# Kernel optimization log

Measured on AMD Instinct MI355X. Metric: run time of the kernel, lower is better.

## Reference

```python
import jax, jax.numpy as jnp
import numpy as np

B, N, D, RNN, K_TOPK = 32, 2000, 128, 640, 64


def setup_inputs() -> dict:
    key = jax.random.key(0)
    ks = jax.random.split(key, 16)
    s = 1.0 / np.sqrt(D)
    return {
        "Ahat": jax.random.uniform(ks[0], (B, N, N), dtype=jnp.float32),
        "node_embs": jax.random.normal(ks[1], (B, N, D), dtype=jnp.float32),
        "ht": jax.random.normal(ks[2], (B, RNN), dtype=jnp.float32),
        "prev_D": jax.random.normal(ks[3], (B, D, D), dtype=jnp.float32) * s,
        "mapper_w": jax.random.normal(ks[4], (D, RNN), dtype=jnp.float32) / np.sqrt(RNN),
        "mapper_b": jnp.zeros((D,), jnp.float32),
        "Wu": jax.random.normal(ks[5], (D, D), jnp.float32) * s,
        "Uu": jax.random.normal(ks[6], (D, D), jnp.float32) * s,
        "bu": jnp.zeros((D, D), jnp.float32),
        "Wr": jax.random.normal(ks[7], (D, D), jnp.float32) * s,
        "Ur": jax.random.normal(ks[8], (D, D), jnp.float32) * s,
        "br": jnp.zeros((D, D), jnp.float32),
        "Wh": jax.random.normal(ks[9], (D, D), jnp.float32) * s,
        "Uh": jax.random.normal(ks[10], (D, D), jnp.float32) * s,
        "bh": jnp.zeros((D, D), jnp.float32),
        "static_w": jax.random.normal(ks[11], (D, D), jnp.float32) * s,
    }


def _gate(W, U, b, x, h, act):
    # W,U: [D,D]; x,h: [B,D,D]; bias broadcasts over batch
    return act(jnp.einsum('ij,bjk->bik', W, x) + jnp.einsum('ij,bjk->bik', U, h) + b)


def reference(Ahat, node_embs, ht, prev_D, mapper_w, mapper_b,
              Wu, Uu, bu, Wr, Ur, br, Wh, Uh, bh, static_w):
    act = jax.nn.relu
    # ---- TopK_with_h ----
    scorer = jnp.tanh(jax.lax.stop_gradient(ht) @ mapper_w.T + mapper_b)     # [B,D]
    scores = jnp.einsum('bnd,bd->bn', node_embs, scorer)                      # [B,N]
    scores = scores / jnp.linalg.norm(scorer, axis=1, keepdims=True)
    _, topk_idx = jax.lax.top_k(scores, K_TOPK)                               # [B,K_TOPK]
    rep = D // K_TOPK + 1
    idx = jnp.tile(topk_idx, (1, rep))[:, :D]                                 # [B,D] selected node ids
    sel = jnp.take_along_axis(node_embs, idx[:, :, None], axis=1)             # [B,D,Dfeat]
    sel = sel * jnp.tanh(jnp.take_along_axis(scores, idx, axis=1))[..., None]
    logp = jax.nn.log_softmax(scores, axis=1)
    p = jnp.exp(logp)
    entropy = -(p * logp).sum(axis=1)                                         # [B]
    policy_score = jnp.take_along_axis(logp, idx, axis=1).mean(axis=1)        # [B]
    x = sel.transpose(0, 2, 1)                                                # [B,Dfeat,D]
    # ---- mat_GRU_cell: evolve GCN weights ----
    update = _gate(Wu, Uu, bu, x, prev_D, jax.nn.sigmoid)
    reset = _gate(Wr, Ur, br, x, prev_D, jax.nn.sigmoid)
    htilda = _gate(Wh, Uh, bh, x, reset * prev_D, jnp.tanh)
    Dw = (1.0 - update) * prev_D + update * htilda                            # [B,D,D]
    # ---- gather selected subgraph ----
    ne = jnp.take_along_axis(node_embs, idx[:, :, None], axis=1)              # [B,D,Dfeat]
    A = jnp.take_along_axis(Ahat, idx[:, :, None], axis=1)                    # [B,D,N]
    A = jnp.take_along_axis(A, idx[:, None, :], axis=2)                       # [B,D,D]
    di = A.sum(axis=1) ** -0.5                                                # [B,D]
    A = di[:, None, :] * A * jax.lax.stop_gradient(di[:, :, None])
    # ---- GCN with evolved + static weights ----
    h1 = act(jnp.einsum('bkj,bjd->bkd', A, jnp.einsum('bjd,bde->bje', ne, Dw)))
    h2 = act(jnp.einsum('bkj,bjd->bkd', A, jnp.einsum('bjd,de->bje', h1, static_w)))
    out = (h1 + h2) * 0.5                                                     # [B,D,Dfeat]
    return (out, policy_score, scorer, entropy)
```

## Files before the change

kernel.cpp:

```cpp
#include <hip/hip_runtime.h>
#include <math.h>


namespace {
constexpr int B_ = 32;
constexpr int N_ = 2000;
constexpr int D_ = 128;
constexpr int R_ = 640;

constexpr size_t OFF_SCORER = 0;
constexpr size_t OFF_INVN   = 4096;
constexpr size_t OFF_CANDV  = 4128;
constexpr size_t OFF_CANDI  = 20512;
constexpr size_t OFF_STATS  = 36896;
constexpr size_t OFF_TKI    = 37664;
constexpr size_t OFF_T0     = 39712;
constexpr size_t OFF_NE0T   = 41760;
constexpr size_t OFF_A0R    = 303904;
constexpr size_t OFF_DW     = 434976;
constexpr size_t OFF_H1     = 959264;

__global__ __launch_bounds__(1024) void k1_scorer(
    const float* __restrict__ ht, const float* __restrict__ mw,
    const float* __restrict__ mb, float* __restrict__ scorer,
    float* __restrict__ invn, float* __restrict__ outScorer) {
  const int b = blockIdx.x, t = threadIdx.x;
  const int d = t & 127, slice = t >> 7;
  __shared__ float sh[R_];
  __shared__ float part[8][128];
  __shared__ float red[2];
  for (int j = t; j < R_; j += 1024) sh[j] = ht[b * R_ + j];
  __syncthreads();
  const float* wp = mw + (size_t)d * R_ + slice * 80;
  const float* hh = sh + slice * 80;
  float acc = 0.f;
  #pragma unroll
  for (int j = 0; j < 80; j += 4) {
    float4 wv = *reinterpret_cast<const float4*>(wp + j);
    acc += wv.x * hh[j] + wv.y * hh[j + 1] + wv.z * hh[j + 2] + wv.w * hh[j + 3];
  }
  part[slice][d] = acc;
  __syncthreads();
  if (t < 128) {
    float a = mb[t];
    #pragma unroll
    for (int s = 0; s < 8; ++s) a += part[s][t];
    const float sv = tanhf(a);
    scorer[b * D_ + t] = sv;
    outScorer[b * D_ + t] = sv;
    float ss = sv * sv;
    #pragma unroll
    for (int o = 32; o > 0; o >>= 1) ss += __shfl_down(ss, o);
    if ((t & 63) == 0) red[t >> 6] = ss;
  }
  __syncthreads();
  if (t == 0) invn[b] = 1.0f / sqrtf(red[0] + red[1]);
}

__global__ __launch_bounds__(256) void k2_scores(
    const float* __restrict__ node, const float* __restrict__ scorer,
    const float* __restrict__ invn, float* __restrict__ cand_v,
    int* __restrict__ cand_i, float* __restrict__ stats) {
  const int b = blockIdx.x, c = blockIdx.y, t = threadIdx.x;
  const int lane = t & 63, w = t >> 6;
  __shared__ float sc[D_];
  __shared__ float cv[256];
  __shared__ int ci[256];
  __shared__ float r1[4], r2[4];
  if (t < D_) sc[t] = scorer[b * D_ + t];
  __syncthreads();
  const float inv = invn[b];
  const int n = c * 250 + t;
  const bool valid = t < 250;
  float v = -INFINITY;
  if (valid) {
    const float* row = node + ((size_t)b * N_ + n) * D_;
    float acc = 0.f;
    for (int j = 0; j < D_; j += 4) {
      float4 a = *reinterpret_cast<const float4*>(row + j);
      acc += a.x * sc[j] + a.y * sc[j + 1] + a.z * sc[j + 2] + a.w * sc[j + 3];
    }
    v = acc * inv;
  }
  float m = v;
  #pragma unroll
  for (int o = 32; o > 0; o >>= 1) m = fmaxf(m, __shfl_xor(m, o));
  if (lane == 0) r1[w] = m;
  __syncthreads();
  const float Mc = fmaxf(fmaxf(r1[0], r1[1]), fmaxf(r1[2], r1[3]));
  __syncthreads();
  float se = 0.f, sx = 0.f;
  if (valid) {
    const float x = v - Mc;
    const float e = expf(x);
    se = e;
    sx = x * e;
  }
  #pragma unroll
  for (int o = 32; o > 0; o >>= 1) {
    se += __shfl_xor(se, o);
    sx += __shfl_xor(sx, o);
  }
  if (lane == 0) { r1[w] = se; r2[w] = sx; }
  cv[t] = v;
  ci[t] = valid ? n : 0x7fffffff;
  __syncthreads();
  if (t == 0) {
    float* st = stats + ((size_t)b * 8 + c) * 3;
    st[0] = Mc;
    st[1] = r1[0] + r1[1] + r1[2] + r1[3];
    st[2] = r2[0] + r2[1] + r2[2] + r2[3];
  }
  const float mv = cv[t];
  const int mi = ci[t];
  int rank = 0;
  for (int j = 0; j < 256; ++j) {
    const float jv = cv[j];
    const int ji = ci[j];
    rank += (jv > mv || (jv == mv && ji < mi)) ? 1 : 0;
  }
  if (valid && rank < 64) {
    cand_v[((size_t)b * 8 + c) * 64 + rank] = mv;
    cand_i[((size_t)b * 8 + c) * 64 + rank] = mi;
  }
}

__global__ __launch_bounds__(512) void k3_merge(
    const float* __restrict__ cand_v, const int* __restrict__ cand_i,
    const float* __restrict__ stats, const float* __restrict__ node,
    int* __restrict__ tki, float* __restrict__ t0v,
    float* __restrict__ outPolicy, float* __restrict__ outEntropy,
    float* __restrict__ ne0T) {
  const int b = blockIdx.x, t = threadIdx.x;
  __shared__ float cv[512];
  __shared__ int ci[512];
  __shared__ float sv[64];
  __shared__ int si[64];
  __shared__ float lne[64][132];
  cv[t] = cand_v[(size_t)b * 512 + t];
  ci[t] = cand_i[(size_t)b * 512 + t];
  __syncthreads();
  {
    const float mv = cv[t];
    const int mi = ci[t];
    int rank = 0;
    for (int j = 0; j < 512; ++j) {
      const float jv = cv[j];
      const int ji = ci[j];
      rank += (jv > mv || (jv == mv && ji < mi)) ? 1 : 0;
    }
    if (rank < 64) { sv[rank] = mv; si[rank] = mi; }
  }
  __syncthreads();
  if (t < 64) {
    tki[b * 64 + t] = si[t];
    const float v = sv[t];
    t0v[b * 64 + t] = tanhf(v);
    float s = v;
    #pragma unroll
    for (int o = 32; o > 0; o >>= 1) s += __shfl_xor(s, o);
    if (t == 0) {
      float M = -INFINITY;
      for (int c = 0; c < 8; ++c) M = fmaxf(M, stats[((size_t)b * 8 + c) * 3]);
      float se = 0.f, sx = 0.f;
      for (int c = 0; c < 8; ++c) {
        const float* st = stats + ((size_t)b * 8 + c) * 3;
        const float f = expf(st[0] - M);
        se += f * st[1];
        sx += f * (st[2] + (st[0] - M) * st[1]);
      }
      const float logS = logf(se);
      outPolicy[b] = s * (1.0f / 64.0f) - M - logS;
      outEntropy[b] = logS - sx / se;
    }
  }
  __syncthreads();
  {
    const int k = t >> 3, q = t & 7;
    const float* src = node + ((size_t)b * N_ + si[k]) * D_ + q * 16;
    #pragma unroll
    for (int j = 0; j < 16; j += 4)
      *reinterpret_cast<float4*>(&lne[k][q * 16 + j]) =
          *reinterpret_cast<const float4*>(src + j);
  }
  __syncthreads();
  {
    const int f = t >> 2, kh = (t & 3) * 16;
    float* dst = ne0T + ((size_t)b * D_ + f) * 64 + kh;
    #pragma unroll
    for (int j = 0; j < 16; j += 4) {
      float4 vv;
      vv.x = lne[kh + j][f];
      vv.y = lne[kh + j + 1][f];
      vv.z = lne[kh + j + 2][f];
      vv.w = lne[kh + j + 3][f];
      *reinterpret_cast<float4*>(dst + j) = vv;
    }
  }
}

__global__ __launch_bounds__(256) void k4_agather(
    const float* __restrict__ Ahat, const int* __restrict__ tki,
    float* __restrict__ A0r) {
  const int b = blockIdx.x, y = blockIdx.y, t = threadIdx.x;
  __shared__ int idx[64];
  if (t < 64) idx[t] = tki[b * 64 + t];
  __syncthreads();
  const int row = y * 4 + (t >> 6);
  const int col = t & 63;
  A0r[(size_t)b * 4096 + row * 64 + col] =
      Ahat[(size_t)b * N_ * N_ + (size_t)idx[row] * N_ + idx[col]];
}

__global__ __launch_bounds__(256) void k5_gru(
    const float* __restrict__ Wu, const float* __restrict__ Uu, const float* __restrict__ bu,
    const float* __restrict__ Wr, const float* __restrict__ Ur, const float* __restrict__ br,
    const float* __restrict__ Wh, const float* __restrict__ Uh, const float* __restrict__ bh,
    const float* __restrict__ ne0T, const float* __restrict__ t0v,
    const float* __restrict__ P, float* __restrict__ Dw) {
  const int b = blockIdx.x, c = blockIdx.y;
  const int t = threadIdx.x, tx = t & 15, ty = t >> 4;
  __shared__ float Wt[16][132], Ut[16][132];
  __shared__ float Xt[16][17], Yt[16][17];
  __shared__ float gs[2][128][17];
  __shared__ float t0s[16];
  const int col = c * 16 + tx;
  const int kq = col & 63;
  if (t < 16) t0s[t] = t0v[b * 64 + (c & 3) * 16 + t];
  const float* neT = ne0T + (size_t)b * D_ * 64;
  const float* Pb = P + (size_t)b * D_ * D_;
  for (int z = 0; z < 2; ++z) {
    const float* W = z ? Wr : Wu;
    const float* U = z ? Ur : Uu;
    const float* bb = z ? br : bu;
    float acc[8] = {};
    for (int f0 = 0; f0 < D_; f0 += 16) {
      __syncthreads();
      #pragma unroll
      for (int rr = 0; rr < 8; rr++) {
        const int i = rr * 16 + ty;
        Wt[tx][i] = W[i * D_ + f0 + tx];
        Ut[tx][i] = U[i * D_ + f0 + tx];
      }
      Xt[ty][tx] = neT[(f0 + ty) * 64 + kq] * t0s[tx];
      Yt[ty][tx] = Pb[(f0 + ty) * D_ + col];
      __syncthreads();
      #pragma unroll
      for (int ff = 0; ff < 16; ff++) {
        const float xv = Xt[ff][tx];
        const float yv = Yt[ff][tx];
        const float4 wa = *reinterpret_cast<const float4*>(&Wt[ff][ty * 8]);
        const float4 wb = *reinterpret_cast<const float4*>(&Wt[ff][ty * 8 + 4]);
        const float4 ua = *reinterpret_cast<const float4*>(&Ut[ff][ty * 8]);
        const float4 ub = *reinterpret_cast<const float4*>(&Ut[ff][ty * 8 + 4]);
        acc[0] += wa.x * xv + ua.x * yv;
        acc[1] += wa.y * xv + ua.y * yv;
        acc[2] += wa.z * xv + ua.z * yv;
        acc[3] += wa.w * xv + ua.w * yv;
        acc[4] += wb.x * xv + ub.x * yv;
        acc[5] += wb.y * xv + ub.y * yv;
        acc[6] += wb.z * xv + ub.z * yv;
        acc[7] += wb.w * xv + ub.w * yv;
      }
    }
    #pragma unroll
    for (int r = 0; r < 8; r++) {
      const int i = ty * 8 + r;
      const float zz = acc[r] + bb[i * D_ + col];
      gs[z][i][tx] = 1.f / (1.f + expf(-zz));
    }
  }
  float acc[8] = {};
  for (int f0 = 0; f0 < D_; f0 += 16) {
    __syncthreads();
    #pragma unroll
    for (int rr = 0; rr < 8; rr++) {
      const int i = rr * 16 + ty;
      Wt[tx][i] = Wh[i * D_ + f0 + tx];
      Ut[tx][i] = Uh[i * D_ + f0 + tx];
    }
    Xt[ty][tx] = neT[(f0 + ty) * 64 + kq] * t0s[tx];
    Yt[ty][tx] = gs[1][f0 + ty][tx] * Pb[(f0 + ty) * D_ + col];
    __syncthreads();
    #pragma unroll
    for (int ff = 0; ff < 16; ff++) {
      const float xv = Xt[ff][tx];
      const float yv = Yt[ff][tx];
      const float4 wa = *reinterpret_cast<const float4*>(&Wt[ff][ty * 8]);
      const float4 wb = *reinterpret_cast<const float4*>(&Wt[ff][ty * 8 + 4]);
      const float4 ua = *reinterpret_cast<const float4*>(&Ut[ff][ty * 8]);
      const float4 ub = *reinterpret_cast<const float4*>(&Ut[ff][ty * 8 + 4]);
      acc[0] += wa.x * xv + ua.x * yv;
      acc[1] += wa.y * xv + ua.y * yv;
      acc[2] += wa.z * xv + ua.z * yv;
      acc[3] += wa.w * xv + ua.w * yv;
      acc[4] += wb.x * xv + ub.x * yv;
      acc[5] += wb.y * xv + ub.y * yv;
      acc[6] += wb.z * xv + ub.z * yv;
      acc[7] += wb.w * xv + ub.w * yv;
    }
  }
  #pragma unroll
  for (int r = 0; r < 8; r++) {
    const int i = ty * 8 + r;
    const size_t off = ((size_t)b * D_ + i) * D_ + col;
    const float hh = tanhf(acc[r] + bh[i * D_ + col]);
    const float uu = gs[0][i][tx];
    const float pp = Pb[i * D_ + col];
    Dw[off] = (1.f - uu) * pp + uu * hh;
  }
}

__global__ __launch_bounds__(256) void k6_gcn1(
    const float* __restrict__ ne0T, const float* __restrict__ Dw,
    const float* __restrict__ A0r, float* __restrict__ h1ws) {
  const int b = blockIdx.x, c = blockIdx.y;
  const int t = threadIdx.x, tx = t & 15, ty = t >> 4;
  __shared__ float As[64][68];
  __shared__ float di[64];
  __shared__ float At[16][68];
  __shared__ float Bt[16][36];
  __shared__ float Ts[64][36];
  const float* Ab = A0r + (size_t)b * 4096;
  const float* neT = ne0T + (size_t)b * D_ * 64;
  const float* Db = Dw + (size_t)b * D_ * D_;
  #pragma unroll
  for (int ph = 0; ph < 4; ++ph) {
    const int i = ph * 16 + ty;
    *reinterpret_cast<float4*>(&As[i][tx * 4]) =
        *reinterpret_cast<const float4*>(Ab + i * 64 + tx * 4);
  }
  __syncthreads();
  if (t < 64) {
    float s = 0.f;
    #pragma unroll
    for (int i = 0; i < 64; ++i) s += As[i][t];
    di[t] = 1.0f / sqrtf(2.0f * s);
  }
  __syncthreads();
  #pragma unroll
  for (int ph = 0; ph < 4; ++ph) {
    const int i = ph * 16 + ty;
    const float sI = 2.0f * di[i];
    float4 v = *reinterpret_cast<float4*>(&As[i][tx * 4]);
    v.x *= sI * di[tx * 4];
    v.y *= sI * di[tx * 4 + 1];
    v.z *= sI * di[tx * 4 + 2];
    v.w *= sI * di[tx * 4 + 3];
    *reinterpret_cast<float4*>(&As[i][tx * 4]) = v;
  }
  const int colg = t & 7, rowg = t >> 3;
  float acc[2][4] = {};
  for (int f0 = 0; f0 < D_; f0 += 16) {
    __syncthreads();
    {
      const int ff = t >> 4, i4 = (t & 15) * 4;
      *reinterpret_cast<float4*>(&At[ff][i4]) =
          *reinterpret_cast<const float4*>(neT + (f0 + ff) * 64 + i4);
      const int j2 = (t & 15) * 2;
      *reinterpret_cast<float2*>(&Bt[ff][j2]) =
          *reinterpret_cast<const float2*>(Db + (f0 + ff) * D_ + c * 32 + j2);
    }
    __syncthreads();
    #pragma unroll
    for (int ff = 0; ff < 16; ff++) {
      const float a0 = At[ff][rowg * 2];
      const float a1 = At[ff][rowg * 2 + 1];
      const float4 b4 = *reinterpret_cast<const float4*>(&Bt[ff][colg * 4]);
      acc[0][0] += a0 * b4.x; acc[0][1] += a0 * b4.y;
      acc[0][2] += a0 * b4.z; acc[0][3] += a0 * b4.w;
      acc[1][0] += a1 * b4.x; acc[1][1] += a1 * b4.y;
      acc[1][2] += a1 * b4.z; acc[1][3] += a1 * b4.w;
    }
  }
  __syncthreads();
  #pragma unroll
  for (int r = 0; r < 2; r++) {
    float4 o = {acc[r][0], acc[r][1], acc[r][2], acc[r][3]};
    *reinterpret_cast<float4*>(&Ts[rowg * 2 + r][colg * 4]) = o;
  }
  __syncthreads();
  float acc2[2][4] = {};
  for (int ff = 0; ff < 64; ++ff) {
    const float a0 = As[rowg * 2][ff];
    const float a1 = As[rowg * 2 + 1][ff];
    const float4 b4 = *reinterpret_cast<const float4*>(&Ts[ff][colg * 4]);
    acc2[0][0] += a0 * b4.x; acc2[0][1] += a0 * b4.y;
    acc2[0][2] += a0 * b4.z; acc2[0][3] += a0 * b4.w;
    acc2[1][0] += a1 * b4.x; acc2[1][1] += a1 * b4.y;
    acc2[1][2] += a1 * b4.z; acc2[1][3] += a1 * b4.w;
  }
  #pragma unroll
  for (int r = 0; r < 2; r++) {
    float4 o = {fmaxf(acc2[r][0], 0.f), fmaxf(acc2[r][1], 0.f),
                fmaxf(acc2[r][2], 0.f), fmaxf(acc2[r][3], 0.f)};
    *reinterpret_cast<float4*>(h1ws + ((size_t)b * 64 + rowg * 2 + r) * D_ +
                               c * 32 + colg * 4) = o;
  }
}

__global__ __launch_bounds__(256) void k7_gcn2(
    const float* __restrict__ h1ws, const float* __restrict__ sw,
    const float* __restrict__ A0r, float* __restrict__ out) {
  const int b = blockIdx.x, c = blockIdx.y;
  const int t = threadIdx.x, tx = t & 15, ty = t >> 4;
  __shared__ float As[64][68];
  __shared__ float di[64];
  __shared__ float At[16][68];
  __shared__ float Bt[16][36];
  __shared__ float Ts[64][36];
  const float* Ab = A0r + (size_t)b * 4096;
  const float* h1b = h1ws + (size_t)b * 64 * D_;
  #pragma unroll
  for (int ph = 0; ph < 4; ++ph) {
    const int i = ph * 16 + ty;
    *reinterpret_cast<float4*>(&As[i][tx * 4]) =
        *reinterpret_cast<const float4*>(Ab + i * 64 + tx * 4);
  }
  __syncthreads();
  if (t < 64) {
    float s = 0.f;
    #pragma unroll
    for (int i = 0; i < 64; ++i) s += As[i][t];
    di[t] = 1.0f / sqrtf(2.0f * s);
  }
  __syncthreads();
  #pragma unroll
  for (int ph = 0; ph < 4; ++ph) {
    const int i = ph * 16 + ty;
    const float sI = 2.0f * di[i];
    float4 v = *reinterpret_cast<float4*>(&As[i][tx * 4]);
    v.x *= sI * di[tx * 4];
    v.y *= sI * di[tx * 4 + 1];
    v.z *= sI * di[tx * 4 + 2];
    v.w *= sI * di[tx * 4 + 3];
    *reinterpret_cast<float4*>(&As[i][tx * 4]) = v;
  }
  const int colg = t & 7, rowg = t >> 3;
  float acc[2][4] = {};
  for (int f0 = 0; f0 < D_; f0 += 16) {
    __syncthreads();
    {
      const int ff = t >> 4, i4 = (t & 15) * 4;
      #pragma unroll
      for (int s = 0; s < 4; ++s)
        At[ff][i4 + s] = h1b[(i4 + s) * D_ + f0 + ff];
      const int j2 = (t & 15) * 2;
      *reinterpret_cast<float2*>(&Bt[ff][j2]) =
          *reinterpret_cast<const float2*>(sw + (f0 + ff) * D_ + c * 32 + j2);
    }
    __syncthreads();
    #pragma unroll
    for (int ff = 0; ff < 16; ff++) {
      const float a0 = At[ff][rowg * 2];
      const float a1 = At[ff][rowg * 2 + 1];
      const float4 b4 = *reinterpret_cast<const float4*>(&Bt[ff][colg * 4]);
      acc[0][0] += a0 * b4.x; acc[0][1] += a0 * b4.y;
      acc[0][2] += a0 * b4.z; acc[0][3] += a0 * b4.w;
      acc[1][0] += a1 * b4.x; acc[1][1] += a1 * b4.y;
      acc[1][2] += a1 * b4.z; acc[1][3] += a1 * b4.w;
    }
  }
  __syncthreads();
  #pragma unroll
  for (int r = 0; r < 2; r++) {
    float4 o = {acc[r][0], acc[r][1], acc[r][2], acc[r][3]};
    *reinterpret_cast<float4*>(&Ts[rowg * 2 + r][colg * 4]) = o;
  }
  __syncthreads();
  float acc2[2][4] = {};
  for (int ff = 0; ff < 64; ++ff) {
    const float a0 = As[rowg * 2][ff];
    const float a1 = As[rowg * 2 + 1][ff];
    const float4 b4 = *reinterpret_cast<const float4*>(&Ts[ff][colg * 4]);
    acc2[0][0] += a0 * b4.x; acc2[0][1] += a0 * b4.y;
    acc2[0][2] += a0 * b4.z; acc2[0][3] += a0 * b4.w;
    acc2[1][0] += a1 * b4.x; acc2[1][1] += a1 * b4.y;
    acc2[1][2] += a1 * b4.z; acc2[1][3] += a1 * b4.w;
  }
  #pragma unroll
  for (int r = 0; r < 2; r++) {
    const int i = rowg * 2 + r;
    const int k = c * 32 + colg * 4;
    const float4 h1v = *reinterpret_cast<const float4*>(h1b + i * D_ + k);
    float4 o;
    o.x = 0.5f * (h1v.x + fmaxf(acc2[r][0], 0.f));
    o.y = 0.5f * (h1v.y + fmaxf(acc2[r][1], 0.f));
    o.z = 0.5f * (h1v.z + fmaxf(acc2[r][2], 0.f));
    o.w = 0.5f * (h1v.w + fmaxf(acc2[r][3], 0.f));
    *reinterpret_cast<float4*>(out + ((size_t)b * D_ + i) * D_ + k) = o;
    *reinterpret_cast<float4*>(out + ((size_t)b * D_ + i + 64) * D_ + k) = o;
  }
}

}

extern "C" void kernel_launch(void* const* d_in, const int* in_sizes, int n_in,
                              void* d_out, int out_size, void* d_ws, size_t ws_size,
                              hipStream_t stream) {
  (void)in_sizes; (void)n_in; (void)out_size; (void)ws_size;
  const float* Ahat = (const float*)d_in[0];
  const float* node = (const float*)d_in[1];
  const float* ht   = (const float*)d_in[2];
  const float* prevD= (const float*)d_in[3];
  const float* mw   = (const float*)d_in[4];
  const float* mb   = (const float*)d_in[5];
  const float* Wu   = (const float*)d_in[6];
  const float* Uu   = (const float*)d_in[7];
  const float* bu   = (const float*)d_in[8];
  const float* Wr   = (const float*)d_in[9];
  const float* Ur   = (const float*)d_in[10];
  const float* br   = (const float*)d_in[11];
  const float* Wh   = (const float*)d_in[12];
  const float* Uh   = (const float*)d_in[13];
  const float* bh   = (const float*)d_in[14];
  const float* sw   = (const float*)d_in[15];

  float* out = (float*)d_out;
  float* outPolicy  = out + (size_t)B_ * D_ * D_;
  float* outScorer  = outPolicy + B_;
  float* outEntropy = outScorer + (size_t)B_ * D_;

  float* ws = (float*)d_ws;
  float* scorer = ws + OFF_SCORER;
  float* invn   = ws + OFF_INVN;
  float* cand_v = ws + OFF_CANDV;
  int*   cand_i = (int*)(ws + OFF_CANDI);
  float* stats  = ws + OFF_STATS;
  int*   tki    = (int*)(ws + OFF_TKI);
  float* t0v    = ws + OFF_T0;
  float* ne0T   = ws + OFF_NE0T;
  float* A0r    = ws + OFF_A0R;
  float* Dw     = ws + OFF_DW;
  float* h1ws   = ws + OFF_H1;

  k1_scorer<<<B_, 1024, 0, stream>>>(ht, mw, mb, scorer, invn, outScorer);
  k2_scores<<<dim3(B_, 8), 256, 0, stream>>>(node, scorer, invn, cand_v, cand_i, stats);
  k3_merge<<<B_, 512, 0, stream>>>(cand_v, cand_i, stats, node, tki, t0v,
                                   outPolicy, outEntropy, ne0T);
  k4_agather<<<dim3(B_, 16), 256, 0, stream>>>(Ahat, tki, A0r);
  k5_gru<<<dim3(B_, 8), 256, 0, stream>>>(Wu, Uu, bu, Wr, Ur, br, Wh, Uh, bh,
                                          ne0T, t0v, prevD, Dw);
  k6_gcn1<<<dim3(B_, 4), 256, 0, stream>>>(ne0T, Dw, A0r, h1ws);
  k7_gcn2<<<dim3(B_, 4), 256, 0, stream>>>(h1ws, sw, A0r, out);
}
```

Measured before the change: 134.1 us.

## Split per-thread work across more threads and blocks in scoring, merge, GRU and GCN kernels

The scoring kernel now uses 512 threads, splitting each row's dot product and the rank count into two halves combined through shared memory. The merge kernel does the same with 1024 threads. The GRU and GCN kernels halve the output tile per block and double the grid, giving 512 blocks for GRU and 256 for GCN. The goal is to fill more of the GPU's compute units in these small, latency-bound launches. In exchange there is extra shared-memory combining, more barriers, less register reuse per thread, and redundant A-normalisation work in each GCN block.

```diff
diff --git a/kernel.cpp b/kernel.cpp
--- a/kernel.cpp
+++ b/kernel.cpp
@@ -57,40 +57,51 @@
   if (t == 0) invn[b] = 1.0f / sqrtf(red[0] + red[1]);
 }
 
-__global__ __launch_bounds__(256) void k2_scores(
+__global__ __launch_bounds__(512) void k2_scores(
     const float* __restrict__ node, const float* __restrict__ scorer,
     const float* __restrict__ invn, float* __restrict__ cand_v,
     int* __restrict__ cand_i, float* __restrict__ stats) {
   const int b = blockIdx.x, c = blockIdx.y, t = threadIdx.x;
+  const int cand = t & 255, s = t >> 8;
   const int lane = t & 63, w = t >> 6;
   __shared__ float sc[D_];
+  __shared__ float pd[256][2];
   __shared__ float cv[256];
   __shared__ int ci[256];
-  __shared__ float r1[4], r2[4];
+  __shared__ int pr[256][2];
+  __shared__ float r1[8], r2[8];
   if (t < D_) sc[t] = scorer[b * D_ + t];
   __syncthreads();
   const float inv = invn[b];
-  const int n = c * 250 + t;
-  const bool valid = t < 250;
+  const int n = c * 250 + cand;
+  const bool valid = cand < 250;
+  {
+    float acc = 0.f;
+    if (valid) {
+      const float* row = node + ((size_t)b * N_ + n) * D_ + s * 64;
+      const float* scp = sc + s * 64;
+      #pragma unroll
+      for (int j = 0; j < 64; j += 4) {
+        float4 a = *reinterpret_cast<const float4*>(row + j);
+        acc += a.x * scp[j] + a.y * scp[j + 1] + a.z * scp[j + 2] + a.w * scp[j + 3];
+      }
+    }
+    pd[cand][s] = acc;
+  }
+  __syncthreads();
   float v = -INFINITY;
-  if (valid) {
-    const float* row = node + ((size_t)b * N_ + n) * D_;
-    float acc = 0.f;
-    for (int j = 0; j < D_; j += 4) {
-      float4 a = *reinterpret_cast<const float4*>(row + j);
-      acc += a.x * sc[j] + a.y * sc[j + 1] + a.z * sc[j + 2] + a.w * sc[j + 3];
-    }
-    v = acc * inv;
-  }
+  if (s == 0 && valid) v = (pd[cand][0] + pd[cand][1]) * inv;
   float m = v;
   #pragma unroll
   for (int o = 32; o > 0; o >>= 1) m = fmaxf(m, __shfl_xor(m, o));
   if (lane == 0) r1[w] = m;
   __syncthreads();
-  const float Mc = fmaxf(fmaxf(r1[0], r1[1]), fmaxf(r1[2], r1[3]));
+  float Mc = r1[0];
+  #pragma unroll
+  for (int q = 1; q < 8; ++q) Mc = fmaxf(Mc, r1[q]);
   __syncthreads();
   float se = 0.f, sx = 0.f;
-  if (valid) {
+  if (s == 0 && valid) {
     const float x = v - Mc;
     const float e = expf(x);
     se = e;
@@ -102,63 +113,86 @@
     sx += __shfl_xor(sx, o);
   }
   if (lane == 0) { r1[w] = se; r2[w] = sx; }
-  cv[t] = v;
-  ci[t] = valid ? n : 0x7fffffff;
+  if (s == 0) {
+    cv[cand] = v;
+    ci[cand] = valid ? n : 0x7fffffff;
+  }
   __syncthreads();
   if (t == 0) {
+    float Se = 0.f, Sx = 0.f;
+    #pragma unroll
+    for (int q = 0; q < 8; ++q) { Se += r1[q]; Sx += r2[q]; }
     float* st = stats + ((size_t)b * 8 + c) * 3;
     st[0] = Mc;
-    st[1] = r1[0] + r1[1] + r1[2] + r1[3];
-    st[2] = r2[0] + r2[1] + r2[2] + r2[3];
-  }
-  const float mv = cv[t];
-  const int mi = ci[t];
-  int rank = 0;
-  for (int j = 0; j < 256; ++j) {
-    const float jv = cv[j];
-    const int ji = ci[j];
-    rank += (jv > mv || (jv == mv && ji < mi)) ? 1 : 0;
-  }
-  if (valid && rank < 64) {
-    cand_v[((size_t)b * 8 + c) * 64 + rank] = mv;
-    cand_i[((size_t)b * 8 + c) * 64 + rank] = mi;
-  }
-}
-
-__global__ __launch_bounds__(512) void k3_merge(
+    st[1] = Se;
+    st[2] = Sx;
+  }
+  {
+    const float mv = cv[cand];
+    const int mi = ci[cand];
+    int rank = 0;
+    const int j0 = s * 128;
+    for (int j = j0; j < j0 + 128; ++j) {
+      const float jv = cv[j];
+      const int ji = ci[j];
+      rank += (jv > mv || (jv == mv && ji < mi)) ? 1 : 0;
+    }
+    pr[cand][s] = rank;
+  }
+  __syncthreads();
+  if (s == 0 && valid) {
+    const int rk = pr[cand][0] + pr[cand][1];
+    if (rk < 64) {
+      cand_v[((size_t)b * 8 + c) * 64 + rk] = cv[cand];
+      cand_i[((size_t)b * 8 + c) * 64 + rk] = ci[cand];
+    }
+  }
+}
+
+__global__ __launch_bounds__(1024) void k3_merge(
     const float* __restrict__ cand_v, const int* __restrict__ cand_i,
     const float* __restrict__ stats, const float* __restrict__ node,
     int* __restrict__ tki, float* __restrict__ t0v,
     float* __restrict__ outPolicy, float* __restrict__ outEntropy,
     float* __restrict__ ne0T) {
   const int b = blockIdx.x, t = threadIdx.x;
+  const int cand = t & 511, s = t >> 9;
   __shared__ float cv[512];
   __shared__ int ci[512];
+  __shared__ int pr[512][2];
   __shared__ float sv[64];
   __shared__ int si[64];
   __shared__ float lne[64][132];
-  cv[t] = cand_v[(size_t)b * 512 + t];
-  ci[t] = cand_i[(size_t)b * 512 + t];
-  __syncthreads();
-  {
-    const float mv = cv[t];
-    const int mi = ci[t];
+  if (t < 512) {
+    cv[t] = cand_v[(size_t)b * 512 + t];
+    ci[t] = cand_i[(size_t)b * 512 + t];
+  }
+  __syncthreads();
+  {
+    const float mv = cv[cand];
+    const int mi = ci[cand];
     int rank = 0;
-    for (int j = 0; j < 512; ++j) {
+    const int j0 = s * 256;
+    for (int j = j0; j < j0 + 256; ++j) {
       const float jv = cv[j];
       const int ji = ci[j];
       rank += (jv > mv || (jv == mv && ji < mi)) ? 1 : 0;
     }
-    if (rank < 64) { sv[rank] = mv; si[rank] = mi; }
+    pr[cand][s] = rank;
+  }
+  __syncthreads();
+  if (s == 0) {
+    const int rk = pr[cand][0] + pr[cand][1];
+    if (rk < 64) { sv[rk] = cv[cand]; si[rk] = ci[cand]; }
   }
   __syncthreads();
   if (t < 64) {
     tki[b * 64 + t] = si[t];
     const float v = sv[t];
     t0v[b * 64 + t] = tanhf(v);
-    float s = v;
-    #pragma unroll
-    for (int o = 32; o > 0; o >>= 1) s += __shfl_xor(s, o);
+    float sum = v;
+    #pragma unroll
+    for (int o = 32; o > 0; o >>= 1) sum += __shfl_xor(sum, o);
     if (t == 0) {
       float M = -INFINITY;
       for (int c = 0; c < 8; ++c) M = fmaxf(M, stats[((size_t)b * 8 + c) * 3]);
@@ -170,32 +204,30 @@
         sx += f * (st[2] + (st[0] - M) * st[1]);
       }
       const float logS = logf(se);
-      outPolicy[b] = s * (1.0f / 64.0f) - M - logS;
+      outPolicy[b] = sum * (1.0f / 64.0f) - M - logS;
       outEntropy[b] = logS - sx / se;
     }
   }
   __syncthreads();
   {
-    const int k = t >> 3, q = t & 7;
-    const float* src = node + ((size_t)b * N_ + si[k]) * D_ + q * 16;
-    #pragma unroll
-    for (int j = 0; j < 16; j += 4)
-      *reinterpret_cast<float4*>(&lne[k][q * 16 + j]) =
-          *reinterpret_cast<const float4*>(src + j);
-  }
-  __syncthreads();
-  {
-    const int f = t >> 2, kh = (t & 3) * 16;
+    const int k = t >> 4, q = t & 15;
+    const float* src = node + ((size_t)b * N_ + si[k]) * D_ + q * 8;
+    *reinterpret_cast<float4*>(&lne[k][q * 8]) =
+        *reinterpret_cast<const float4*>(src);
+    *reinterpret_cast<float4*>(&lne[k][q * 8 + 4]) =
+        *reinterpret_cast<const float4*>(src + 4);
+  }
+  __syncthreads();
+  {
+    const int f = t >> 3, kh = (t & 7) * 8;
     float* dst = ne0T + ((size_t)b * D_ + f) * 64 + kh;
-    #pragma unroll
-    for (int j = 0; j < 16; j += 4) {
-      float4 vv;
-      vv.x = lne[kh + j][f];
-      vv.y = lne[kh + j + 1][f];
-      vv.z = lne[kh + j + 2][f];
-      vv.w = lne[kh + j + 3][f];
-      *reinterpret_cast<float4*>(dst + j) = vv;
-    }
+    float4 a, bq;
+    a.x = lne[kh][f];     a.y = lne[kh + 1][f];
+    a.z = lne[kh + 2][f]; a.w = lne[kh + 3][f];
+    bq.x = lne[kh + 4][f]; bq.y = lne[kh + 5][f];
+    bq.z = lne[kh + 6][f]; bq.w = lne[kh + 7][f];
+    *reinterpret_cast<float4*>(dst) = a;
+    *reinterpret_cast<float4*>(dst + 4) = bq;
   }
 }
 
@@ -219,90 +251,86 @@
     const float* __restrict__ ne0T, const float* __restrict__ t0v,
     const float* __restrict__ P, float* __restrict__ Dw) {
   const int b = blockIdx.x, c = blockIdx.y;
-  const int t = threadIdx.x, tx = t & 15, ty = t >> 4;
+  const int t = threadIdx.x;
+  const int tx = t & 7, ty = t >> 3;
+  const int sx_ = t & 15, sy_ = t >> 4;
   __shared__ float Wt[16][132], Ut[16][132];
-  __shared__ float Xt[16][17], Yt[16][17];
-  __shared__ float gs[2][128][17];
-  __shared__ float t0s[16];
-  const int col = c * 16 + tx;
-  const int kq = col & 63;
-  if (t < 16) t0s[t] = t0v[b * 64 + (c & 3) * 16 + t];
+  __shared__ float Xt[16][9], Yt[16][9];
+  __shared__ float gs[2][128][9];
+  __shared__ float t0s[8];
+  const int col = c * 8 + tx;
+  const int kq = (c & 7) * 8 + tx;
+  if (t < 8) t0s[t] = t0v[b * 64 + (c & 7) * 8 + t];
   const float* neT = ne0T + (size_t)b * D_ * 64;
   const float* Pb = P + (size_t)b * D_ * D_;
   for (int z = 0; z < 2; ++z) {
     const float* W = z ? Wr : Wu;
     const float* U = z ? Ur : Uu;
     const float* bb = z ? br : bu;
-    float acc[8] = {};
+    float acc[4] = {};
     for (int f0 = 0; f0 < D_; f0 += 16) {
       __syncthreads();
       #pragma unroll
       for (int rr = 0; rr < 8; rr++) {
-        const int i = rr * 16 + ty;
-        Wt[tx][i] = W[i * D_ + f0 + tx];
-        Ut[tx][i] = U[i * D_ + f0 + tx];
+        const int i = rr * 16 + sy_;
+        Wt[sx_][i] = W[i * D_ + f0 + sx_];
+        Ut[sx_][i] = U[i * D_ + f0 + sx_];
       }
-      Xt[ty][tx] = neT[(f0 + ty) * 64 + kq] * t0s[tx];
-      Yt[ty][tx] = Pb[(f0 + ty) * D_ + col];
+      if (t < 128) {
+        const int ff = t >> 3, kk = t & 7;
+        Xt[ff][kk] = neT[(f0 + ff) * 64 + (c & 7) * 8 + kk] * t0s[kk];
+        Yt[ff][kk] = Pb[(f0 + ff) * D_ + c * 8 + kk];
+      }
       __syncthreads();
       #pragma unroll
       for (int ff = 0; ff < 16; ff++) {
         const float xv = Xt[ff][tx];
         const float yv = Yt[ff][tx];
-        const float4 wa = *reinterpret_cast<const float4*>(&Wt[ff][ty * 8]);
-        const float4 wb = *reinterpret_cast<const float4*>(&Wt[ff][ty * 8 + 4]);
-        const float4 ua = *reinterpret_cast<const float4*>(&Ut[ff][ty * 8]);
-        const float4 ub = *reinterpret_cast<const float4*>(&Ut[ff][ty * 8 + 4]);
+        const float4 wa = *reinterpret_cast<const float4*>(&Wt[ff][ty * 4]);
+        const float4 ua = *reinterpret_cast<const float4*>(&Ut[ff][ty * 4]);
         acc[0] += wa.x * xv + ua.x * yv;
         acc[1] += wa.y * xv + ua.y * yv;
         acc[2] += wa.z * xv + ua.z * yv;
         acc[3] += wa.w * xv + ua.w * yv;
-        acc[4] += wb.x * xv + ub.x * yv;
-        acc[5] += wb.y * xv + ub.y * yv;
-        acc[6] += wb.z * xv + ub.z * yv;
-        acc[7] += wb.w * xv + ub.w * yv;
       }
     }
     #pragma unroll
-    for (int r = 0; r < 8; r++) {
-      const int i = ty * 8 + r;
+    for (int r = 0; r < 4; r++) {
+      const int i = ty * 4 + r;
       const float zz = acc[r] + bb[i * D_ + col];
       gs[z][i][tx] = 1.f / (1.f + expf(-zz));
     }
   }
-  float acc[8] = {};
+  float acc[4] = {};
   for (int f0 = 0; f0 < D_; f0 += 16) {
     __syncthreads();
     #pragma unroll
     for (int rr = 0; rr < 8; rr++) {
-      const int i = rr * 16 + ty;
-      Wt[tx][i] = Wh[i * D_ + f0 + tx];
-      Ut[tx][i] = Uh[i * D_ + f0 + tx];
-    }
-    Xt[ty][tx] = neT[(f0 + ty) * 64 + kq] * t0s[tx];
-    Yt[ty][tx] = gs[1][f0 + ty][tx] * Pb[(f0 + ty) * D_ + col];
+      const int i = rr * 16 + sy_;
+      Wt[sx_][i] = Wh[i * D_ + f0 + sx_];
+      Ut[sx_][i] = Uh[i * D_ + f0 + sx_];
+    }
+    if (t < 128) {
+      const int ff = t >> 3, kk = t & 7;
+      Xt[ff][kk] = neT[(f0 + ff) * 64 + (c & 7) * 8 + kk] * t0s[kk];
+      Yt[ff][kk] = gs[1][f0 + ff][kk] * Pb[(f0 + ff) * D_ + c * 8 + kk];
+    }
     __syncthreads();
     #pragma unroll
     for (int ff = 0; ff < 16; ff++) {
       const float xv = Xt[ff][tx];
       const float yv = Yt[ff][tx];
-      const float4 wa = *reinterpret_cast<const float4*>(&Wt[ff][ty * 8]);
-      const float4 wb = *reinterpret_cast<const float4*>(&Wt[ff][ty * 8 + 4]);
-      const float4 ua = *reinterpret_cast<const float4*>(&Ut[ff][ty * 8]);
-      const float4 ub = *reinterpret_cast<const float4*>(&Ut[ff][ty * 8 + 4]);
+      const float4 wa = *reinterpret_cast<const float4*>(&Wt[ff][ty * 4]);
+      const float4 ua = *reinterpret_cast<const float4*>(&Ut[ff][ty * 4]);
       acc[0] += wa.x * xv + ua.x * yv;
       acc[1] += wa.y * xv + ua.y * yv;
       acc[2] += wa.z * xv + ua.z * yv;
       acc[3] += wa.w * xv + ua.w * yv;
-      acc[4] += wb.x * xv + ub.x * yv;
-      acc[5] += wb.y * xv + ub.y * yv;
-      acc[6] += wb.z * xv + ub.z * yv;
-      acc[7] += wb.w * xv + ub.w * yv;
-    }
-  }
-  #pragma unroll
-  for (int r = 0; r < 8; r++) {
-    const int i = ty * 8 + r;
+    }
+  }
+  #pragma unroll
+  for (int r = 0; r < 4; r++) {
+    const int i = ty * 4 + r;
     const size_t off = ((size_t)b * D_ + i) * D_ + col;
     const float hh = tanhf(acc[r] + bh[i * D_ + col]);
     const float uu = gs[0][i][tx];
@@ -315,12 +343,14 @@
     const float* __restrict__ ne0T, const float* __restrict__ Dw,
     const float* __restrict__ A0r, float* __restrict__ h1ws) {
   const int b = blockIdx.x, c = blockIdx.y;
-  const int t = threadIdx.x, tx = t & 15, ty = t >> 4;
+  const int t = threadIdx.x;
+  const int tx = t & 15, ty = t >> 4;
+  const int colg = t & 3, rowg = t >> 2;
   __shared__ float As[64][68];
   __shared__ float di[64];
   __shared__ float At[16][68];
-  __shared__ float Bt[16][36];
-  __shared__ float Ts[64][36];
+  __shared__ float Bt[16][20];
+  __shared__ float Ts[64][20];
   const float* Ab = A0r + (size_t)b * 4096;
   const float* neT = ne0T + (size_t)b * D_ * 64;
   const float* Db = Dw + (size_t)b * D_ * D_;
@@ -349,53 +379,45 @@
     v.w *= sI * di[tx * 4 + 3];
     *reinterpret_cast<float4*>(&As[i][tx * 4]) = v;
   }
-  const int colg = t & 7, rowg = t >> 3;
-  float acc[2][4] = {};
+  float acc[4] = {};
   for (int f0 = 0; f0 < D_; f0 += 16) {
     __syncthreads();
     {
-      const int ff = t >> 4, i4 = (t & 15) * 4;
-      *reinterpret_cast<float4*>(&At[ff][i4]) =
-          *reinterpret_cast<const float4*>(neT + (f0 + ff) * 64 + i4);
-      const int j2 = (t & 15) * 2;
-      *reinterpret_cast<float2*>(&Bt[ff][j2]) =
-          *reinterpret_cast<const float2*>(Db + (f0 + ff) * D_ + c * 32 + j2);
+      *reinterpret_cast<float4*>(&At[ty][tx * 4]) =
+          *reinterpret_cast<const float4*>(neT + (f0 + ty) * 64 + tx * 4);
+      Bt[ty][tx] = Db[(f0 + ty) * D_ + c * 16 + tx];
     }
     __syncthreads();
     #pragma unroll
     for (int ff = 0; ff < 16; ff++) {
-      const float a0 = At[ff][rowg * 2];
-      const float a1 = At[ff][rowg * 2 + 1];
+      const float a = At[ff][rowg];
       const float4 b4 = *reinterpret_cast<const float4*>(&Bt[ff][colg * 4]);
-      acc[0][0] += a0 * b4.x; acc[0][1] += a0 * b4.y;
-      acc[0][2] += a0 * b4.z; acc[0][3] += a0 * b4.w;
-      acc[1][0] += a1 * b4.x; acc[1][1] += a1 * b4.y;
-      acc[1][2] += a1 * b4.z; acc[1][3] += a1 * b4.w;
-    }
-  }
-  __syncthreads();
-  #pragma unroll
-  for (int r = 0; r < 2; r++) {
-    float4 o = {acc[r][0], acc[r][1], acc[r][2], acc[r][3]};
-    *reinterpret_cast<float4*>(&Ts[rowg * 2 + r][colg * 4]) = o;
-  }
-  __syncthreads();
-  float acc2[2][4] = {};
+      acc[0] += a * b4.x;
+      acc[1] += a * b4.y;
+      acc[2] += a * b4.z;
+      acc[3] += a * b4.w;
+    }
+  }
+  __syncthreads();
+  {
+    float4 o = {acc[0], acc[1], acc[2], acc[3]};
+    *reinterpret_cast<float4*>(&Ts[rowg][colg * 4]) = o;
+  }
+  __syncthreads();
+  float acc2[4] = {};
   for (int ff = 0; ff < 64; ++ff) {
-    const float a0 = As[rowg * 2][ff];
-    const float a1 = As[rowg * 2 + 1][ff];
+    const float a = As[rowg][ff];
     const float4 b4 = *reinterpret_cast<const float4*>(&Ts[ff][colg * 4]);
-    acc2[0][0] += a0 * b4.x; acc2[0][1] += a0 * b4.y;
-    acc2[0][2] += a0 * b4.z; acc2[0][3] += a0 * b4.w;
-    acc2[1][0] += a1 * b4.x; acc2[1][1] += a1 * b4.y;
-    acc2[1][2] += a1 * b4.z; acc2[1][3] += a1 * b4.w;
-  }
-  #pragma unroll
-  for (int r = 0; r < 2; r++) {
-    float4 o = {fmaxf(acc2[r][0], 0.f), fmaxf(acc2[r][1], 0.f),
-                fmaxf(acc2[r][2], 0.f), fmaxf(acc2[r][3], 0.f)};
-    *reinterpret_cast<float4*>(h1ws + ((size_t)b * 64 + rowg * 2 + r) * D_ +
-                               c * 32 + colg * 4) = o;
+    acc2[0] += a * b4.x;
+    acc2[1] += a * b4.y;
+    acc2[2] += a * b4.z;
+    acc2[3] += a * b4.w;
+  }
+  {
+    float4 o = {fmaxf(acc2[0], 0.f), fmaxf(acc2[1], 0.f),
+                fmaxf(acc2[2], 0.f), fmaxf(acc2[3], 0.f)};
+    *reinterpret_cast<float4*>(h1ws + ((size_t)b * 64 + rowg) * D_ +
+                               c * 16 + colg * 4) = o;
   }
 }
 
@@ -403,12 +425,14 @@
     const float* __restrict__ h1ws, const float* __restrict__ sw,
     const float* __restrict__ A0r, float* __restrict__ out) {
   const int b = blockIdx.x, c = blockIdx.y;
-  const int t = threadIdx.x, tx = t & 15, ty = t >> 4;
+  const int t = threadIdx.x;
+  const int tx = t & 15, ty = t >> 4;
+  const int colg = t & 3, rowg = t >> 2;
   __shared__ float As[64][68];
   __shared__ float di[64];
   __shared__ float At[16][68];
-  __shared__ float Bt[16][36];
-  __shared__ float Ts[64][36];
+  __shared__ float Bt[16][20];
+  __shared__ float Ts[64][20];
   const float* Ab = A0r + (size_t)b * 4096;
   const float* h1b = h1ws + (size_t)b * 64 * D_;
   #pragma unroll
@@ -436,60 +460,52 @@
     v.w *= sI * di[tx * 4 + 3];
     *reinterpret_cast<float4*>(&As[i][tx * 4]) = v;
   }
-  const int colg = t & 7, rowg = t >> 3;
-  float acc[2][4] = {};
+  float acc[4] = {};
   for (int f0 = 0; f0 < D_; f0 += 16) {
     __syncthreads();
     {
-      const int ff = t >> 4, i4 = (t & 15) * 4;
+      const int i4 = tx * 4;
       #pragma unroll
       for (int s = 0; s < 4; ++s)
-        At[ff][i4 + s] = h1b[(i4 + s) * D_ + f0 + ff];
-      const int j2 = (t & 15) * 2;
-      *reinterpret_cast<float2*>(&Bt[ff][j2]) =
-          *reinterpret_cast<const float2*>(sw + (f0 + ff) * D_ + c * 32 + j2);
+        At[ty][i4 + s] = h1b[(i4 + s) * D_ + f0 + ty];
+      Bt[ty][tx] = sw[(f0 + ty) * D_ + c * 16 + tx];
     }
     __syncthreads();
     #pragma unroll
     for (int ff = 0; ff < 16; ff++) {
-      const float a0 = At[ff][rowg * 2];
-      const float a1 = At[ff][rowg * 2 + 1];
+      const float a = At[ff][rowg];
       const float4 b4 = *reinterpret_cast<const float4*>(&Bt[ff][colg * 4]);
-      acc[0][0] += a0 * b4.x; acc[0][1] += a0 * b4.y;
-      acc[0][2] += a0 * b4.z; acc[0][3] += a0 * b4.w;
-      acc[1][0] += a1 * b4.x; acc[1][1] += a1 * b4.y;
-      acc[1][2] += a1 * b4.z; acc[1][3] += a1 * b4.w;
-    }
-  }
-  __syncthreads();
-  #pragma unroll
-  for (int r = 0; r < 2; r++) {
-    float4 o = {acc[r][0], acc[r][1], acc[r][2], acc[r][3]};
-    *reinterpret_cast<float4*>(&Ts[rowg * 2 + r][colg * 4]) = o;
-  }
-  __syncthreads();
-  float acc2[2][4] = {};
+      acc[0] += a * b4.x;
+      acc[1] += a * b4.y;
+      acc[2] += a * b4.z;
+      acc[3] += a * b4.w;
+    }
+  }
+  __syncthreads();
+  {
+    float4 o = {acc[0], acc[1], acc[2], acc[3]};
+    *reinterpret_cast<float4*>(&Ts[rowg][colg * 4]) = o;
+  }
+  __syncthreads();
+  float acc2[4] = {};
   for (int ff = 0; ff < 64; ++ff) {
-    const float a0 = As[rowg * 2][ff];
-    const float a1 = As[rowg * 2 + 1][ff];
+    const float a = As[rowg][ff];
     const float4 b4 = *reinterpret_cast<const float4*>(&Ts[ff][colg * 4]);
-    acc2[0][0] += a0 * b4.x; acc2[0][1] += a0 * b4.y;
-    acc2[0][2] += a0 * b4.z; acc2[0][3] += a0 * b4.w;
-    acc2[1][0] += a1 * b4.x; acc2[1][1] += a1 * b4.y;
-    acc2[1][2] += a1 * b4.z; acc2[1][3] += a1 * b4.w;
-  }
-  #pragma unroll
-  for (int r = 0; r < 2; r++) {
-    const int i = rowg * 2 + r;
-    const int k = c * 32 + colg * 4;
-    const float4 h1v = *reinterpret_cast<const float4*>(h1b + i * D_ + k);
+    acc2[0] += a * b4.x;
+    acc2[1] += a * b4.y;
+    acc2[2] += a * b4.z;
+    acc2[3] += a * b4.w;
+  }
+  {
+    const int k = c * 16 + colg * 4;
+    const float4 h1v = *reinterpret_cast<const float4*>(h1b + rowg * D_ + k);
     float4 o;
-    o.x = 0.5f * (h1v.x + fmaxf(acc2[r][0], 0.f));
-    o.y = 0.5f * (h1v.y + fmaxf(acc2[r][1], 0.f));
-    o.z = 0.5f * (h1v.z + fmaxf(acc2[r][2], 0.f));
-    o.w = 0.5f * (h1v.w + fmaxf(acc2[r][3], 0.f));
-    *reinterpret_cast<float4*>(out + ((size_t)b * D_ + i) * D_ + k) = o;
-    *reinterpret_cast<float4*>(out + ((size_t)b * D_ + i + 64) * D_ + k) = o;
+    o.x = 0.5f * (h1v.x + fmaxf(acc2[0], 0.f));
+    o.y = 0.5f * (h1v.y + fmaxf(acc2[1], 0.f));
+    o.z = 0.5f * (h1v.z + fmaxf(acc2[2], 0.f));
+    o.w = 0.5f * (h1v.w + fmaxf(acc2[3], 0.f));
+    *reinterpret_cast<float4*>(out + ((size_t)b * D_ + rowg) * D_ + k) = o;
+    *reinterpret_cast<float4*>(out + ((size_t)b * D_ + rowg + 64) * D_ + k) = o;
   }
 }
 
@@ -535,12 +551,12 @@
   float* h1ws   = ws + OFF_H1;
 
   k1_scorer<<<B_, 1024, 0, stream>>>(ht, mw, mb, scorer, invn, outScorer);
-  k2_scores<<<dim3(B_, 8), 256, 0, stream>>>(node, scorer, invn, cand_v, cand_i, stats);
-  k3_merge<<<B_, 512, 0, stream>>>(cand_v, cand_i, stats, node, tki, t0v,
-                                   outPolicy, outEntropy, ne0T);
+  k2_scores<<<dim3(B_, 8), 512, 0, stream>>>(node, scorer, invn, cand_v, cand_i, stats);
+  k3_merge<<<B_, 1024, 0, stream>>>(cand_v, cand_i, stats, node, tki, t0v,
+                                    outPolicy, outEntropy, ne0T);
   k4_agather<<<dim3(B_, 16), 256, 0, stream>>>(Ahat, tki, A0r);
-  k5_gru<<<dim3(B_, 8), 256, 0, stream>>>(Wu, Uu, bu, Wr, Ur, br, Wh, Uh, bh,
-                                          ne0T, t0v, prevD, Dw);
-  k6_gcn1<<<dim3(B_, 4), 256, 0, stream>>>(ne0T, Dw, A0r, h1ws);
-  k7_gcn2<<<dim3(B_, 4), 256, 0, stream>>>(h1ws, sw, A0r, out);
-}
+  k5_gru<<<dim3(B_, 16), 256, 0, stream>>>(Wu, Uu, bu, Wr, Ur, br, Wh, Uh, bh,
+                                           ne0T, t0v, prevD, Dw);
+  k6_gcn1<<<dim3(B_, 8), 256, 0, stream>>>(ne0T, Dw, A0r, h1ws);
+  k7_gcn2<<<dim3(B_, 8), 256, 0, stream>>>(h1ws, sw, A0r, out);
+}
```

Result: faster. 123.3 us (-8.1%).
